# Kernel optimization log

Hardware: AMD Instinct MI355X
Metric: run time of the kernel (lower is better)

Reference implementation:

```python
import jax, jax.numpy as jnp
import numpy as np

B, C, HD, H, W = 4, 64, 64, 64, 64  # batch, input_dim, hidden_dim, spatial


def conv1x1(x, w, b):
    # x: [B, Cin, H, W], w: [Cout, Cin], b: [Cout]
    return jnp.einsum('oc,bchw->bohw', w, x) + b[None, :, None, None]


def setup_inputs() -> dict:
    key = jax.random.key(0)
    ks = jax.random.split(key, 16)
    sc = lambda cin: 1.0 / np.sqrt(cin)
    d = {
        'h': jax.random.normal(ks[0], (B, C, H, W), jnp.float32),
        'm': jax.random.normal(ks[1], (B, C, H, W), jnp.float32),
        'Wq': jax.random.normal(ks[2], (HD, C), jnp.float32) * sc(C),
        'bq': jnp.zeros((HD,), jnp.float32),
        'Wk': jax.random.normal(ks[3], (HD, C), jnp.float32) * sc(C),
        'bk': jnp.zeros((HD,), jnp.float32),
        'Wk2': jax.random.normal(ks[4], (HD, C), jnp.float32) * sc(C),
        'bk2': jnp.zeros((HD,), jnp.float32),
        'Wv': jax.random.normal(ks[5], (C, C), jnp.float32) * sc(C),
        'bv': jnp.zeros((C,), jnp.float32),
        'Wv2': jax.random.normal(ks[6], (C, C), jnp.float32) * sc(C),
        'bv2': jnp.zeros((C,), jnp.float32),
        'Wz': jax.random.normal(ks[7], (2 * C, 2 * C), jnp.float32) * sc(2 * C),
        'bz': jnp.zeros((2 * C,), jnp.float32),
        'Wm': jax.random.normal(ks[8], (3 * C, 3 * C), jnp.float32) * sc(3 * C),
        'bm': jnp.zeros((3 * C,), jnp.float32),
    }
    return d


def reference(h, m, Wq, bq, Wk, bk, Wk2, bk2, Wv, bv, Wv2, bv2, Wz, bz, Wm, bm):
    b, c, hh, ww = h.shape
    n = hh * ww
    K_h = conv1x1(h, Wk, bk).reshape(b, HD, n)            # [B, HD, N]
    Q_h = conv1x1(h, Wq, bq).reshape(b, HD, n).transpose(0, 2, 1)  # [B, N, HD]
    V_h = conv1x1(h, Wv, bv).reshape(b, c, n)             # [B, C, N]
    K_m = conv1x1(m, Wk2, bk2).reshape(b, HD, n)
    V_m = conv1x1(m, Wv2, bv2).reshape(b, c, n)

    A_h = jax.nn.softmax(jnp.einsum('bnd,bdk->bnk', Q_h, K_h), axis=-1)  # [B, N, N]
    Z_h = jnp.einsum('bnk,bck->bcn', A_h, V_h).reshape(b, c, hh, ww)
    A_m = jax.nn.softmax(jnp.einsum('bnd,bdk->bnk', Q_h, K_m), axis=-1)
    Z_m = jnp.einsum('bnk,bck->bcn', A_m, V_m).reshape(b, c, hh, ww)

    Z = conv1x1(jnp.concatenate([Z_h, Z_m], axis=1), Wz, bz)   # [B, 2C, H, W]
    combined = conv1x1(jnp.concatenate([Z, h], axis=1), Wm, bm)  # [B, 3C, H, W]
    mo, mg, mi = jnp.split(combined, 3, axis=1)
    mi = jax.nn.sigmoid(mi)
    new_m = (1.0 - mi) * m + mi * jnp.tanh(mg)
    new_h = jax.nn.sigmoid(mo) * new_m
    return (new_h, new_m)
```

## Files before the change

kernel.cpp:

```cpp
#include <hip/hip_runtime.h>

#define BN 4
#define NN 4096
#define SPLITK 2
#define LOG2E 1.44269504f
#define MFIX 36.0f

typedef __attribute__((ext_vector_type(8))) __bf16 bf16x8;
typedef __attribute__((ext_vector_type(4))) short s16x4;
typedef __attribute__((ext_vector_type(4))) float f32x4;
typedef unsigned short u16;

__device__ __forceinline__ u16 f2bf(float x) {
  unsigned int u = __builtin_bit_cast(unsigned int, x);
  u = (u + 0x7fffu + ((u >> 16) & 1u)) >> 16;
  return (u16)u;
}
__device__ __forceinline__ u16 f2bfs(float x) {
  __bf16 b = (__bf16)x;
  return __builtin_bit_cast(u16, b);
}
__device__ __forceinline__ float bf2f(u16 s) {
  unsigned int u = ((unsigned int)s) << 16;
  return __builtin_bit_cast(float, u);
}

__device__ __forceinline__ f32x4 mfma16(s16x4 a, s16x4 b, f32x4 c) {
#if defined(__HIP_DEVICE_COMPILE__)
  return __builtin_amdgcn_mfma_f32_16x16x16bf16_1k(a, b, c, 0, 0, 0);
#else
  return c;
#endif
}

__device__ __forceinline__ void gld16(const u16* g, u16* l) {
#if defined(__HIP_DEVICE_COMPILE__)
  __builtin_amdgcn_global_load_lds(
      (const __attribute__((address_space(1))) void*)g,
      (__attribute__((address_space(3))) void*)l, 16, 0, 0);
#else
  (void)g; (void)l;
#endif
}

#define PACK16(A, P0, P1)                                                          \
    P0.x = (unsigned)f2bf(A[0]) | ((unsigned)f2bf(A[1]) << 16);                    \
    P0.y = (unsigned)f2bf(A[2]) | ((unsigned)f2bf(A[3]) << 16);                    \
    P0.z = (unsigned)f2bf(A[4]) | ((unsigned)f2bf(A[5]) << 16);                    \
    P0.w = (unsigned)f2bf(A[6]) | ((unsigned)f2bf(A[7]) << 16);                    \
    P1.x = (unsigned)f2bf(A[8]) | ((unsigned)f2bf(A[9]) << 16);                    \
    P1.y = (unsigned)f2bf(A[10]) | ((unsigned)f2bf(A[11]) << 16);                  \
    P1.z = (unsigned)f2bf(A[12]) | ((unsigned)f2bf(A[13]) << 16);                  \
    P1.w = (unsigned)f2bf(A[14]) | ((unsigned)f2bf(A[15]) << 16);

__global__ __launch_bounds__(256) void fuse_w2_kernel(
    const float* __restrict__ Wz, const float* __restrict__ bz,
    const float* __restrict__ Wm, const float* __restrict__ bm,
    u16* __restrict__ Wbig, float* __restrict__ bbig) {
  __shared__ float wrow[128];
  __shared__ float bzs[128];
  int o = blockIdx.x;
  int t = threadIdx.x;
  if (t < 128) { wrow[t] = Wm[o * 192 + t]; bzs[t] = bz[t]; }
  __syncthreads();
  if (t < 128) {
    float s = 0.f;
#pragma unroll 4
    for (int j = 0; j < 128; ++j) s = fmaf(wrow[j], Wz[j * 128 + t], s);
    Wbig[o * 192 + t] = f2bf(s);
  } else if (t < 192) {
    Wbig[o * 192 + t] = f2bf(Wm[o * 192 + t]);
  } else if (t == 192) {
    float s = bm[o];
    for (int j = 0; j < 128; ++j) s = fmaf(wrow[j], bzs[j], s);
    bbig[o] = s;
  }
}

__global__ __launch_bounds__(256) void proj2_kernel(
    const float* __restrict__ h, const float* __restrict__ m,
    const float* __restrict__ Wq, const float* __restrict__ bq,
    const float* __restrict__ Wk, const float* __restrict__ bk,
    const float* __restrict__ Wk2, const float* __restrict__ bk2,
    const float* __restrict__ Wv, const float* __restrict__ bv,
    const float* __restrict__ Wv2, const float* __restrict__ bv2,
    u16* __restrict__ Q, u16* __restrict__ Kh, u16* __restrict__ Km,
    u16* __restrict__ Vh, u16* __restrict__ Vm, u16* __restrict__ hT) {
  __shared__ float xs[64][65];
  int blk = blockIdx.x;
  int ntile = blk & 63, b = (blk >> 6) & 3, pid = blk >> 8;
  int n0 = ntile * 64;
  int t = threadIdx.x, nl = t & 63;
  const float* src = (pid == 2 || pid == 4) ? m : h;
  {
    int c0 = (t >> 6) * 16;
#pragma unroll
    for (int i = 0; i < 16; ++i) {
      int c = c0 + i;
      xs[c][nl] = src[((size_t)(b * 64) + c) * NN + n0 + nl];
    }
  }
  __syncthreads();
  int w = __builtin_amdgcn_readfirstlane(t >> 6);
  size_t nrow = (size_t)b * NN + n0 + nl;
  float acc[16];
  if (pid == 5) {
#pragma unroll
    for (int i = 0; i < 16; ++i) acc[i] = xs[w * 16 + i][nl];
  } else {
    const float* W = pid == 0 ? Wq : pid == 1 ? Wk : pid == 2 ? Wk2 : pid == 3 ? Wv : Wv2;
    const float* bs = pid == 0 ? bq : pid == 1 ? bk : pid == 2 ? bk2 : pid == 3 ? bv : bv2;
#pragma unroll
    for (int i = 0; i < 16; ++i) acc[i] = bs[w * 16 + i];
    for (int c = 0; c < 64; ++c) {
      float x = xs[c][nl];
#pragma unroll
      for (int i = 0; i < 16; ++i) acc[i] = fmaf(W[(w * 16 + i) * 64 + c], x, acc[i]);
    }
    if (pid == 0) {
#pragma unroll
      for (int i = 0; i < 16; ++i) acc[i] *= LOG2E;
    }
  }
  if (pid == 3 || pid == 4) {
    u16* dst = (pid == 3) ? Vh : Vm;
#pragma unroll
    for (int i = 0; i < 16; ++i) {
      int o = w * 16 + i;
      dst[((size_t)(b * 64) + o) * NN + n0 + nl] = f2bf(acc[i]);
    }
  } else {
    u16* dst = pid == 0 ? Q : pid == 1 ? Kh : pid == 2 ? Km : hT;
    uint4 p0, p1;
    PACK16(acc, p0, p1);
    uint4* dp = (uint4*)(dst + nrow * 64 + w * 16);
    dp[0] = p0; dp[1] = p1;
  }
}

__global__ __launch_bounds__(256, 2) void flash9_kernel(
    const u16* __restrict__ Qg, const u16* __restrict__ Khg,
    const u16* __restrict__ Kmg, const u16* __restrict__ Vhg,
    const u16* __restrict__ Vmg, u16* __restrict__ Opart,
    float* __restrict__ Lpart) {
  __shared__ u16 Kl[2][8192];
  __shared__ u16 Vl[2][8192];
  int blk = blockIdx.x;
  int combo = blk & 15, qt = blk >> 4;
  int attn = combo & 1, b = (combo >> 1) & 3, split = combo >> 3;
  const u16* K = (attn ? Kmg : Khg) + (size_t)b * NN * 64;
  const u16* V = (attn ? Vmg : Vhg) + (size_t)b * 64 * NN;
  int t = threadIdx.x, wave = t >> 6, lane = t & 63, col = lane & 15, quad = lane >> 4;
  int row0 = qt * 128 + wave * 32;

  bf16x8 bq[2][2];
#pragma unroll
  for (int g = 0; g < 2; ++g) {
    const u16* qp = Qg + (size_t)b * NN * 64 + (size_t)(row0 + g * 16 + col) * 64 + quad * 8;
    bq[g][0] = *(const bf16x8*)(const void*)qp;
    bq[g][1] = *(const bf16x8*)(const void*)(qp + 32);
  }

  f32x4 O[2][4];
#pragma unroll
  for (int g = 0; g < 2; ++g)
#pragma unroll
    for (int i = 0; i < 4; ++i) O[g][i] = f32x4{0.f, 0.f, 0.f, 0.f};
  f32x4 Lacc[2];
  Lacc[0] = f32x4{0.f, 0.f, 0.f, 0.f};
  Lacc[1] = f32x4{0.f, 0.f, 0.f, 0.f};
  s16x4 ones;
#pragma unroll
  for (int i = 0; i < 4; ++i) ones[i] = (short)0x3F80;
  int sp8 = split * 8 + b * 2 + attn;

  const int kbase = split * (NN / SPLITK);
  const int TILES = NN / SPLITK / 128;

#define STAGE(BUF, K0)                                                           \
  _Pragma("unroll") for (int jj = 0; jj < 4; ++jj) {                             \
    int p = jj * 256 + t;                                                        \
    int krow_ = p >> 3;                                                          \
    int kj_ = (p & 7) ^ (krow_ & 7);                                             \
    gld16(K + (size_t)((K0) + krow_) * 64 + kj_ * 8, &Kl[BUF][p * 8]);           \
    int vrow_ = p >> 4;                                                          \
    int vj_ = (p & 15) ^ (vrow_ & 7);                                            \
    gld16(V + (size_t)vrow_ * NN + (K0) + vj_ * 8, &Vl[BUF][p * 8]);             \
  }

  STAGE(0, kbase);

  for (int kt = 0; kt < TILES; ++kt) {
    __syncthreads();
    int cur = kt & 1;
    if (kt + 1 < TILES) { STAGE(cur ^ 1, kbase + (kt + 1) * 128); }
    const u16* Kb = &Kl[cur][0];
    const u16* Vb = &Vl[cur][0];
    f32x4 St[8][2];
#pragma unroll
    for (int nt = 0; nt < 8; ++nt) {
      int row = nt * 16 + col;
      int ph0 = row * 8 + (quad ^ (col & 7));
      int ph1 = row * 8 + ((4 + quad) ^ (col & 7));
      bf16x8 a0 = *(const bf16x8*)(const void*)(Kb + ph0 * 8);
      bf16x8 a1 = *(const bf16x8*)(const void*)(Kb + ph1 * 8);
#pragma unroll
      for (int g = 0; g < 2; ++g) {
        f32x4 acc = {-MFIX, -MFIX, -MFIX, -MFIX};
        acc = __builtin_amdgcn_mfma_f32_16x16x32_bf16(a0, bq[g][0], acc, 0, 0, 0);
        acc = __builtin_amdgcn_mfma_f32_16x16x32_bf16(a1, bq[g][1], acc, 0, 0, 0);
        St[nt][g] = acc;
      }
    }
    s16x4 pfrag[8][2];
#pragma unroll
    for (int nt = 0; nt < 8; ++nt)
#pragma unroll
      for (int g = 0; g < 2; ++g) {
        s16x4 pf;
#pragma unroll
        for (int r = 0; r < 4; ++r)
          pf[r] = (short)f2bfs(__builtin_exp2f(St[nt][g][r]));
        pfrag[nt][g] = pf;
        Lacc[g] = mfma16(pf, ones, Lacc[g]);
      }
#pragma unroll
    for (int nt = 0; nt < 8; ++nt) {
      int j = nt * 2 + (quad >> 1);
#pragma unroll
      for (int ct = 0; ct < 4; ++ct) {
        int c = ct * 16 + col;
        int ph = c * 16 + (j ^ (c & 7));
        s16x4 vf = *(const s16x4*)(const void*)(Vb + ph * 8 + (quad & 1) * 4);
        O[0][ct] = mfma16(pfrag[nt][0], vf, O[0][ct]);
        O[1][ct] = mfma16(pfrag[nt][1], vf, O[1][ct]);
      }
    }
  }
#undef STAGE

#pragma unroll
  for (int g = 0; g < 2; ++g) {
#pragma unroll
    for (int ct = 0; ct < 4; ++ct)
#pragma unroll
      for (int r = 0; r < 4; ++r) {
        size_t q = (size_t)row0 + g * 16 + quad * 4 + r;
        Opart[((size_t)sp8 * NN + q) * 64 + ct * 16 + col] = f2bfs(O[g][ct][r]);
      }
    if (col == 0) {
#pragma unroll
      for (int r = 0; r < 4; ++r)
        Lpart[(size_t)sp8 * NN + row0 + g * 16 + quad * 4 + r] = Lacc[g][r];
    }
  }
}

__global__ __launch_bounds__(256) void epi3_kernel(
    const u16* __restrict__ Wb, const float* __restrict__ bb,
    const u16* __restrict__ Opart, const float* __restrict__ Lpart,
    const u16* __restrict__ hT, const float* __restrict__ mglob,
    float* __restrict__ out) {
  int blk = blockIdx.x;
  int ng = blk * 16;
  int b = ng >> 12;
  int t = threadIdx.x, wave = t >> 6, lane = t & 63, col = lane & 15, quad = lane >> 4;
  int qb = (ng & (NN - 1)) + col;
  int s0h = b * 2, s1h = 8 + b * 2, s0m = b * 2 + 1, s1m = 9 + b * 2;
  float invLh = 1.f / (Lpart[(size_t)s0h * NN + qb] + Lpart[(size_t)s1h * NN + qb]);
  float invLm = 1.f / (Lpart[(size_t)s0m * NN + qb] + Lpart[(size_t)s1m * NN + qb]);
  size_t nrow = ((size_t)ng + col) * 64;
  bf16x8 bfr[6];
#define MERGEF(DST, SP0, SP1, OFF, INVL)                                         \
  {                                                                              \
    const u16* p0_ = Opart + ((size_t)(SP0) * NN + qb) * 64 + (OFF);             \
    const u16* p1_ = Opart + ((size_t)(SP1) * NN + qb) * 64 + (OFF);             \
    bf16x8 a_ = *(const bf16x8*)(const void*)p0_;                                \
    bf16x8 c_ = *(const bf16x8*)(const void*)p1_;                                \
    bf16x8 r_;                                                                   \
    _Pragma("unroll") for (int i = 0; i < 8; ++i)                                \
      r_[i] = (__bf16)(((float)a_[i] + (float)c_[i]) * (INVL));                  \
    DST = r_;                                                                    \
  }
  MERGEF(bfr[0], s0h, s1h, quad * 8, invLh);
  MERGEF(bfr[1], s0h, s1h, 32 + quad * 8, invLh);
  MERGEF(bfr[2], s0m, s1m, quad * 8, invLm);
  MERGEF(bfr[3], s0m, s1m, 32 + quad * 8, invLm);
#undef MERGEF
  bfr[4] = *(const bf16x8*)(const void*)(hT + nrow + quad * 8);
  bfr[5] = *(const bf16x8*)(const void*)(hT + nrow + 32 + quad * 8);
  f32x4 acc[3];
#pragma unroll
  for (int j = 0; j < 3; ++j) {
    int mt = wave + j * 4;
#pragma unroll
    for (int r = 0; r < 4; ++r) acc[j][r] = bb[mt * 16 + quad * 4 + r];
  }
#pragma unroll
  for (int ks = 0; ks < 6; ++ks) {
#pragma unroll
    for (int j = 0; j < 3; ++j) {
      int mt = wave + j * 4;
      bf16x8 af = *(const bf16x8*)(const void*)(Wb + (size_t)(mt * 16 + col) * 192 + ks * 32 + quad * 8);
      acc[j] = __builtin_amdgcn_mfma_f32_16x16x32_bf16(af, bfr[ks], acc[j], 0, 0, 0);
    }
  }
  int nloc = (ng & (NN - 1)) + col;
#pragma unroll
  for (int r = 0; r < 4; ++r) {
    int o = wave * 16 + quad * 4 + r;
    float mo = acc[0][r], mgt = acc[1][r], mi = acc[2][r];
    float si = 1.f / (1.f + __builtin_exp2f(-mi * LOG2E));
    float tg = 1.f - 2.f / (__builtin_exp2f(2.f * LOG2E * mgt) + 1.f);
    float mv = mglob[(size_t)(b * 64 + o) * NN + nloc];
    float nm = (1.f - si) * mv + si * tg;
    float nh = nm / (1.f + __builtin_exp2f(-mo * LOG2E));
    out[(size_t)(b * 64 + o) * NN + nloc] = nh;
    out[(size_t)BN * 64 * NN + (size_t)(b * 64 + o) * NN + nloc] = nm;
  }
}

extern "C" void kernel_launch(void* const* d_in, const int* in_sizes, int n_in,
                              void* d_out, int out_size, void* d_ws, size_t ws_size,
                              hipStream_t stream) {
  const float* h = (const float*)d_in[0];
  const float* m = (const float*)d_in[1];
  const float* Wq = (const float*)d_in[2];
  const float* bq = (const float*)d_in[3];
  const float* Wk = (const float*)d_in[4];
  const float* bk = (const float*)d_in[5];
  const float* Wk2 = (const float*)d_in[6];
  const float* bk2 = (const float*)d_in[7];
  const float* Wv = (const float*)d_in[8];
  const float* bv = (const float*)d_in[9];
  const float* Wv2 = (const float*)d_in[10];
  const float* bv2 = (const float*)d_in[11];
  const float* Wz = (const float*)d_in[12];
  const float* bz = (const float*)d_in[13];
  const float* Wm = (const float*)d_in[14];
  const float* bm = (const float*)d_in[15];
  float* out = (float*)d_out;

  size_t off = 0;
  auto alloc = [&](size_t bytes) {
    void* p = (char*)d_ws + off;
    off += (bytes + 255) & ~(size_t)255;
    return p;
  };
  const size_t bn64 = (size_t)BN * NN * 64;
  u16* Q  = (u16*)alloc(bn64 * 2);
  u16* Kh = (u16*)alloc(bn64 * 2);
  u16* Km = (u16*)alloc(bn64 * 2);
  u16* Vh = (u16*)alloc(bn64 * 2);
  u16* Vm = (u16*)alloc(bn64 * 2);
  u16* hT = (u16*)alloc(bn64 * 2);
  u16* Opart = (u16*)alloc((size_t)SPLITK * 8 * NN * 64 * 2);
  float* Lpart = (float*)alloc((size_t)SPLITK * 8 * NN * 4);
  u16* Wbigbf = (u16*)alloc(192 * 192 * 2);
  float* bbig = (float*)alloc(192 * 4);
  (void)ws_size; (void)in_sizes; (void)n_in; (void)out_size;

  fuse_w2_kernel<<<192, 256, 0, stream>>>(Wz, bz, Wm, bm, Wbigbf, bbig);
  proj2_kernel<<<6 * BN * 64, 256, 0, stream>>>(h, m, Wq, bq, Wk, bk, Wk2, bk2, Wv, bv,
                                                Wv2, bv2, Q, Kh, Km, Vh, Vm, hT);
  flash9_kernel<<<512, 256, 0, stream>>>(Q, Kh, Km, Vh, Vm, Opart, Lpart);
  epi3_kernel<<<(BN * NN) / 16, 256, 0, stream>>>(Wbigbf, bbig, Opart, Lpart, hT, m, out);
}
```

Measured before the change: 197.0 us.

## Pre-swizzle V into MFMA fragment layout, stage projection weights in LDS, use native exp2

The projection kernel now writes V in a blocked layout that matches the MFMA B-fragment order, so the attention kernel can stage V with contiguous loads and read fragments without XOR address math. Projection weights are copied into shared memory once per block instead of being read from global memory inside the inner loop. exp2 calls switch to the hardware intrinsic, and the score accumulator init becomes a hoisted constant. The new V layout must stay consistent between producer and consumer, and the raw exp2 intrinsic may handle edge cases differently from the library call.

```diff
diff --git a/kernel.cpp b/kernel.cpp
--- a/kernel.cpp
+++ b/kernel.cpp
@@ -23,6 +23,14 @@
 __device__ __forceinline__ float bf2f(u16 s) {
   unsigned int u = ((unsigned int)s) << 16;
   return __builtin_bit_cast(float, u);
+}
+
+__device__ __forceinline__ float fexp2(float x) {
+#if defined(__HIP_DEVICE_COMPILE__) && __has_builtin(__builtin_amdgcn_exp2f)
+  return __builtin_amdgcn_exp2f(x);
+#else
+  return __builtin_exp2f(x);
+#endif
 }
 
 __device__ __forceinline__ f32x4 mfma16(s16x4 a, s16x4 b, f32x4 c) {
@@ -77,7 +85,7 @@
   }
 }
 
-__global__ __launch_bounds__(256) void proj2_kernel(
+__global__ __launch_bounds__(256) void proj3_kernel(
     const float* __restrict__ h, const float* __restrict__ m,
     const float* __restrict__ Wq, const float* __restrict__ bq,
     const float* __restrict__ Wk, const float* __restrict__ bk,
@@ -87,6 +95,7 @@
     u16* __restrict__ Q, u16* __restrict__ Kh, u16* __restrict__ Km,
     u16* __restrict__ Vh, u16* __restrict__ Vm, u16* __restrict__ hT) {
   __shared__ float xs[64][65];
+  __shared__ float Wl[4096];
   int blk = blockIdx.x;
   int ntile = blk & 63, b = (blk >> 6) & 3, pid = blk >> 8;
   int n0 = ntile * 64;
@@ -100,6 +109,11 @@
       xs[c][nl] = src[((size_t)(b * 64) + c) * NN + n0 + nl];
     }
   }
+  if (pid < 5) {
+    const float* W = pid == 0 ? Wq : pid == 1 ? Wk : pid == 2 ? Wk2 : pid == 3 ? Wv : Wv2;
+#pragma unroll
+    for (int i = 0; i < 16; ++i) Wl[i * 256 + t] = W[i * 256 + t];
+  }
   __syncthreads();
   int w = __builtin_amdgcn_readfirstlane(t >> 6);
   size_t nrow = (size_t)b * NN + n0 + nl;
@@ -108,14 +122,13 @@
 #pragma unroll
     for (int i = 0; i < 16; ++i) acc[i] = xs[w * 16 + i][nl];
   } else {
-    const float* W = pid == 0 ? Wq : pid == 1 ? Wk : pid == 2 ? Wk2 : pid == 3 ? Wv : Wv2;
     const float* bs = pid == 0 ? bq : pid == 1 ? bk : pid == 2 ? bk2 : pid == 3 ? bv : bv2;
 #pragma unroll
     for (int i = 0; i < 16; ++i) acc[i] = bs[w * 16 + i];
     for (int c = 0; c < 64; ++c) {
       float x = xs[c][nl];
 #pragma unroll
-      for (int i = 0; i < 16; ++i) acc[i] = fmaf(W[(w * 16 + i) * 64 + c], x, acc[i]);
+      for (int i = 0; i < 16; ++i) acc[i] = fmaf(Wl[(w * 16 + i) * 64 + c], x, acc[i]);
     }
     if (pid == 0) {
 #pragma unroll
@@ -124,11 +137,11 @@
   }
   if (pid == 3 || pid == 4) {
     u16* dst = (pid == 3) ? Vh : Vm;
-#pragma unroll
-    for (int i = 0; i < 16; ++i) {
-      int o = w * 16 + i;
-      dst[((size_t)(b * 64) + o) * NN + n0 + nl] = f2bf(acc[i]);
-    }
+    int key = n0 + nl;
+    size_t base = ((size_t)b << 18) + (size_t)(key >> 4) * 1024 + w * 256 +
+                  ((key >> 2) & 3) * 64 + (key & 3);
+#pragma unroll
+    for (int i = 0; i < 16; ++i) dst[base + i * 4] = f2bf(acc[i]);
   } else {
     u16* dst = pid == 0 ? Q : pid == 1 ? Kh : pid == 2 ? Km : hT;
     uint4 p0, p1;
@@ -138,7 +151,7 @@
   }
 }
 
-__global__ __launch_bounds__(256, 2) void flash9_kernel(
+__global__ __launch_bounds__(256, 2) void flash10_kernel(
     const u16* __restrict__ Qg, const u16* __restrict__ Khg,
     const u16* __restrict__ Kmg, const u16* __restrict__ Vhg,
     const u16* __restrict__ Vmg, u16* __restrict__ Opart,
@@ -149,7 +162,7 @@
   int combo = blk & 15, qt = blk >> 4;
   int attn = combo & 1, b = (combo >> 1) & 3, split = combo >> 3;
   const u16* K = (attn ? Kmg : Khg) + (size_t)b * NN * 64;
-  const u16* V = (attn ? Vmg : Vhg) + (size_t)b * 64 * NN;
+  const u16* V = (attn ? Vmg : Vhg) + ((size_t)b << 18);
   int t = threadIdx.x, wave = t >> 6, lane = t & 63, col = lane & 15, quad = lane >> 4;
   int row0 = qt * 128 + wave * 32;
 
@@ -169,6 +182,7 @@
   f32x4 Lacc[2];
   Lacc[0] = f32x4{0.f, 0.f, 0.f, 0.f};
   Lacc[1] = f32x4{0.f, 0.f, 0.f, 0.f};
+  const f32x4 minit = {-MFIX, -MFIX, -MFIX, -MFIX};
   s16x4 ones;
 #pragma unroll
   for (int i = 0; i < 4; ++i) ones[i] = (short)0x3F80;
@@ -183,9 +197,7 @@
     int krow_ = p >> 3;                                                          \
     int kj_ = (p & 7) ^ (krow_ & 7);                                             \
     gld16(K + (size_t)((K0) + krow_) * 64 + kj_ * 8, &Kl[BUF][p * 8]);           \
-    int vrow_ = p >> 4;                                                          \
-    int vj_ = (p & 15) ^ (vrow_ & 7);                                            \
-    gld16(V + (size_t)vrow_ * NN + (K0) + vj_ * 8, &Vl[BUF][p * 8]);             \
+    gld16(V + (size_t)(K0) * 64 + p * 8, &Vl[BUF][p * 8]);                       \
   }
 
   STAGE(0, kbase);
@@ -206,8 +218,7 @@
       bf16x8 a1 = *(const bf16x8*)(const void*)(Kb + ph1 * 8);
 #pragma unroll
       for (int g = 0; g < 2; ++g) {
-        f32x4 acc = {-MFIX, -MFIX, -MFIX, -MFIX};
-        acc = __builtin_amdgcn_mfma_f32_16x16x32_bf16(a0, bq[g][0], acc, 0, 0, 0);
+        f32x4 acc = __builtin_amdgcn_mfma_f32_16x16x32_bf16(a0, bq[g][0], minit, 0, 0, 0);
         acc = __builtin_amdgcn_mfma_f32_16x16x32_bf16(a1, bq[g][1], acc, 0, 0, 0);
         St[nt][g] = acc;
       }
@@ -219,19 +230,16 @@
       for (int g = 0; g < 2; ++g) {
         s16x4 pf;
 #pragma unroll
-        for (int r = 0; r < 4; ++r)
-          pf[r] = (short)f2bfs(__builtin_exp2f(St[nt][g][r]));
+        for (int r = 0; r < 4; ++r) pf[r] = (short)f2bfs(fexp2(St[nt][g][r]));
         pfrag[nt][g] = pf;
         Lacc[g] = mfma16(pf, ones, Lacc[g]);
       }
+    const u16* vbase = Vb + quad * 64 + col * 4;
 #pragma unroll
     for (int nt = 0; nt < 8; ++nt) {
-      int j = nt * 2 + (quad >> 1);
 #pragma unroll
       for (int ct = 0; ct < 4; ++ct) {
-        int c = ct * 16 + col;
-        int ph = c * 16 + (j ^ (c & 7));
-        s16x4 vf = *(const s16x4*)(const void*)(Vb + ph * 8 + (quad & 1) * 4);
+        s16x4 vf = *(const s16x4*)(const void*)(vbase + nt * 1024 + ct * 256);
         O[0][ct] = mfma16(pfrag[nt][0], vf, O[0][ct]);
         O[1][ct] = mfma16(pfrag[nt][1], vf, O[1][ct]);
       }
@@ -310,11 +318,11 @@
   for (int r = 0; r < 4; ++r) {
     int o = wave * 16 + quad * 4 + r;
     float mo = acc[0][r], mgt = acc[1][r], mi = acc[2][r];
-    float si = 1.f / (1.f + __builtin_exp2f(-mi * LOG2E));
-    float tg = 1.f - 2.f / (__builtin_exp2f(2.f * LOG2E * mgt) + 1.f);
+    float si = 1.f / (1.f + fexp2(-mi * LOG2E));
+    float tg = 1.f - 2.f / (fexp2(2.f * LOG2E * mgt) + 1.f);
     float mv = mglob[(size_t)(b * 64 + o) * NN + nloc];
     float nm = (1.f - si) * mv + si * tg;
-    float nh = nm / (1.f + __builtin_exp2f(-mo * LOG2E));
+    float nh = nm / (1.f + fexp2(-mo * LOG2E));
     out[(size_t)(b * 64 + o) * NN + nloc] = nh;
     out[(size_t)BN * 64 * NN + (size_t)(b * 64 + o) * NN + nloc] = nm;
   }
@@ -361,8 +369,8 @@
   (void)ws_size; (void)in_sizes; (void)n_in; (void)out_size;
 
   fuse_w2_kernel<<<192, 256, 0, stream>>>(Wz, bz, Wm, bm, Wbigbf, bbig);
-  proj2_kernel<<<6 * BN * 64, 256, 0, stream>>>(h, m, Wq, bq, Wk, bk, Wk2, bk2, Wv, bv,
+  proj3_kernel<<<6 * BN * 64, 256, 0, stream>>>(h, m, Wq, bq, Wk, bk, Wk2, bk2, Wv, bv,
                                                 Wv2, bv2, Q, Kh, Km, Vh, Vm, hT);
-  flash9_kernel<<<512, 256, 0, stream>>>(Q, Kh, Km, Vh, Vm, Opart, Lpart);
+  flash10_kernel<<<512, 256, 0, stream>>>(Q, Kh, Km, Vh, Vm, Opart, Lpart);
   epi3_kernel<<<(BN * NN) / 16, 256, 0, stream>>>(Wbigbf, bbig, Opart, Lpart, hT, m, out);
 }
```

New measurement: 175.8 us. 1.12x faster.
